# Kernel optimization log

Hardware: AMD Instinct MI355X
Metric: run time of the kernel (lower is better)

The kernel has to match this reference:

```python
import jax, jax.numpy as jnp
import numpy as np

B, G, F = 256, 2048, 128   # batch, graph_size, feat_size (== gcn_dim == k)
RNN_DIM = 512
K = F  # self.k = args.gcn_dim


def setup_inputs() -> dict:
    key = jax.random.key(0)
    k1, k2, k3 = jax.random.split(key, 3)
    node_embs = jax.random.normal(k1, (B, G, F), dtype=jnp.float32)
    mask = jnp.zeros((B, G), dtype=jnp.float32)
    h_t = jax.random.normal(k2, (B, RNN_DIM), dtype=jnp.float32)
    W_map = jax.random.normal(k3, (RNN_DIM, F), dtype=jnp.float32) * (1.0 / np.sqrt(RNN_DIM))
    b_map = jnp.zeros((F,), dtype=jnp.float32)
    return {"node_embs": node_embs, "mask": mask, "h_t": h_t, "W_map": W_map, "b_map": b_map}


def reference(node_embs, mask, h_t, W_map, b_map):
    # mapper: Linear + Tanh -> scorer [B, F]
    scorer = jnp.tanh(h_t @ W_map + b_map)
    # scores = bmm(node_embs, scorer) / ||scorer||  -> [B, G]
    norm = jnp.linalg.norm(scorer, axis=1, keepdims=True)  # [B, 1]
    scores = jnp.einsum('bgf,bf->bg', node_embs, scorer) / norm
    scores = scores + mask
    # top-k over graph dim (mask is all-zero so no -inf filtering/padding needed)
    vals, topk_indices = jax.lax.top_k(scores, K)  # [B, K]
    # gather node embeddings at topk indices, scale by tanh of gathered scores
    gathered = jnp.take_along_axis(node_embs, topk_indices[:, :, None], axis=1)  # [B, K, F]
    out = gathered * jnp.tanh(vals)[:, :, None]  # tanh(scores.gather) == tanh(vals)
    # log-softmax over graph dim, gather at topk, mean -> policy score [B]
    log_probs = jax.nn.log_softmax(scores, axis=-1)
    score = jnp.take_along_axis(log_probs, topk_indices, axis=-1)  # [B, K]
    policy_score = score.mean(axis=1)
    return (jnp.transpose(out, (0, 2, 1)), policy_score)  # ([B, F, K], [B])
```

## Files before the change

kernel.cpp:

```cpp
#include <hip/hip_runtime.h>
#include <cmath>

#define B_ 256
#define G_ 2048
#define F_ 128
#define RNN_ 512
#define K_ 128

__global__ __launch_bounds__(128) void k_scorer(const float* __restrict__ h_t,
                                                const float* __restrict__ W,
                                                const float* __restrict__ b_map,
                                                float* __restrict__ scorer_norm) {
    __shared__ float h[RNN_];
    __shared__ float red[128];
    const int b = blockIdx.x;
    const int f = threadIdx.x;
    for (int i = f; i < RNN_; i += 128) h[i] = h_t[b * RNN_ + i];
    __syncthreads();
    float acc = 0.f;
#pragma unroll 8
    for (int r = 0; r < RNN_; ++r) acc += h[r] * W[r * F_ + f];
    const float t = tanhf(acc + b_map[f]);
    red[f] = t * t;
    __syncthreads();
    for (int s = 64; s > 0; s >>= 1) {
        if (f < s) red[f] += red[f + s];
        __syncthreads();
    }
    const float norm = sqrtf(red[0]);
    scorer_norm[b * F_ + f] = t / norm;
}

__global__ __launch_bounds__(256) void k_scores(const float* __restrict__ node,
                                                const float* __restrict__ mask,
                                                const float* __restrict__ scorer_norm,
                                                float* __restrict__ scores) {
    const int b = blockIdx.y;
    const int gbase = blockIdx.x * 64;
    const int tid = threadIdx.x;
    const int wave = tid >> 6;
    const int lane = tid & 63;
    const int half = lane >> 5;
    const int l32 = lane & 31;

    const float4 s4 = ((const float4*)(scorer_norm + b * F_))[l32];
    const float4* nb = (const float4*)(node + (size_t)b * G_ * F_);
    const int rowbase = gbase + wave * 16;
#pragma unroll
    for (int p = 0; p < 8; ++p) {
        const int g = rowbase + p * 2 + half;
        const float4 e = nb[(size_t)g * 32 + l32];
        float part = e.x * s4.x + e.y * s4.y + e.z * s4.z + e.w * s4.w;
        part += __shfl_xor(part, 16);
        part += __shfl_xor(part, 8);
        part += __shfl_xor(part, 4);
        part += __shfl_xor(part, 2);
        part += __shfl_xor(part, 1);
        if (l32 == 0) scores[b * G_ + g] = part + mask[b * G_ + g];
    }
}

__global__ __launch_bounds__(512) void k_topk(const float* __restrict__ node,
                                              const float* __restrict__ scores,
                                              float* __restrict__ out,
                                              float* __restrict__ policy) {
    __shared__ float sc[G_];
    __shared__ unsigned long long keys[G_];
    __shared__ float tile[K_][33];
    __shared__ float tanhv[K_];
    __shared__ int idxk[K_];
    __shared__ float valk[K_];
    __shared__ float red[512];

    const int b = blockIdx.x;
    const int tid = threadIdx.x;

    for (int i = tid; i < G_; i += 512) {
        const float v = scores[b * G_ + i];
        sc[i] = v;
        unsigned u = __float_as_uint(v);
        u = (u & 0x80000000u) ? ~u : (u | 0x80000000u);
        keys[i] = ((unsigned long long)u << 32) | (unsigned)(G_ - 1 - i);
    }
    __syncthreads();

    for (int k = 2; k <= G_; k <<= 1) {
        for (int j = k >> 1; j > 0; j >>= 1) {
            for (int i = tid; i < G_; i += 512) {
                const int ij = i ^ j;
                if (ij > i) {
                    const unsigned long long a = keys[i], c = keys[ij];
                    const bool up = ((i & k) == 0);
                    if (up ? (a > c) : (a < c)) {
                        keys[i] = c;
                        keys[ij] = a;
                    }
                }
            }
            __syncthreads();
        }
    }

    if (tid < K_) {
        const unsigned long long key = keys[G_ - 1 - tid];
        const int idx = G_ - 1 - (int)(unsigned)(key & 0xFFFFFFFFull);
        idxk[tid] = idx;
        const float v = sc[idx];
        valk[tid] = v;
        tanhv[tid] = tanhf(v);
    }
    __syncthreads();

    const float maxv = sc[G_ - 1 - (int)(unsigned)(keys[G_ - 1] & 0xFFFFFFFFull)];
    float s = 0.f;
    for (int i = tid; i < G_; i += 512) s += expf(sc[i] - maxv);
    red[tid] = s;
    __syncthreads();
    for (int o = 256; o > 0; o >>= 1) {
        if (tid < o) red[tid] += red[tid + o];
        __syncthreads();
    }
    const float lse = maxv + logf(red[0]);
    if (tid == 0) {
        float sum = 0.f;
        for (int k2 = 0; k2 < K_; ++k2) sum += valk[k2];
        policy[b] = sum * (1.0f / K_) - lse;
    }

    const float* nb = node + (size_t)b * G_ * F_;
    float* ob = out + (size_t)b * F_ * K_;
    for (int f0 = 0; f0 < F_; f0 += 32) {
        for (int e = tid; e < K_ * 32; e += 512) {
            const int k2 = e >> 5;
            const int f = e & 31;
            tile[k2][f] = nb[(size_t)idxk[k2] * F_ + f0 + f];
        }
        __syncthreads();
        for (int e = tid; e < 32 * K_; e += 512) {
            const int f = e >> 7;
            const int k2 = e & 127;
            ob[(size_t)(f0 + f) * K_ + k2] = tile[k2][f] * tanhv[k2];
        }
        __syncthreads();
    }
}

extern "C" void kernel_launch(void* const* d_in, const int* in_sizes, int n_in,
                              void* d_out, int out_size, void* d_ws, size_t ws_size,
                              hipStream_t stream) {
    const float* node = (const float*)d_in[0];
    const float* mask = (const float*)d_in[1];
    const float* h_t = (const float*)d_in[2];
    const float* W = (const float*)d_in[3];
    const float* bm = (const float*)d_in[4];

    float* out = (float*)d_out;
    float* policy = out + (size_t)B_ * F_ * K_;

    float* scorer_norm = (float*)d_ws;
    float* scores = scorer_norm + B_ * F_;

    k_scorer<<<B_, 128, 0, stream>>>(h_t, W, bm, scorer_norm);
    k_scores<<<dim3(G_ / 64, B_), 256, 0, stream>>>(node, mask, scorer_norm, scores);
    k_topk<<<B_, 512, 0, stream>>>(node, scores, out, policy);
}
```

Measured before the change: 454.5 us.

## Replace full bitonic sort with radix-select threshold plus small sort of top-k

The top-k kernel no longer bitonic-sorts all 2048 keys. It runs an 8-pass radix select with per-wave shared histograms to find the exact k-th key, compacts the 128 winners with an atomic counter, and bitonic-sorts only those. The scorer kernel splits the RNN reduction across 512 threads in four partial sums, and the gather loads node rows as float4. The aim is to cut the O(G log² G) sort work and barriers, at the cost of eight histogram passes that each need several syncs.

```diff
diff --git a/kernel.cpp b/kernel.cpp
--- a/kernel.cpp
+++ b/kernel.cpp
@@ -7,28 +7,37 @@
 #define RNN_ 512
 #define K_ 128
 
-__global__ __launch_bounds__(128) void k_scorer(const float* __restrict__ h_t,
+__global__ __launch_bounds__(512) void k_scorer(const float* __restrict__ h_t,
                                                 const float* __restrict__ W,
                                                 const float* __restrict__ b_map,
                                                 float* __restrict__ scorer_norm) {
     __shared__ float h[RNN_];
-    __shared__ float red[128];
+    __shared__ float part[4][F_];
+    __shared__ float red[F_];
     const int b = blockIdx.x;
-    const int f = threadIdx.x;
-    for (int i = f; i < RNN_; i += 128) h[i] = h_t[b * RNN_ + i];
-    __syncthreads();
+    const int tid = threadIdx.x;
+    h[tid] = h_t[b * RNN_ + tid];
+    __syncthreads();
+    const int f = tid & 127;
+    const int qu = tid >> 7;
     float acc = 0.f;
+    const int r0 = qu * (RNN_ / 4);
 #pragma unroll 8
-    for (int r = 0; r < RNN_; ++r) acc += h[r] * W[r * F_ + f];
-    const float t = tanhf(acc + b_map[f]);
-    red[f] = t * t;
+    for (int r = r0; r < r0 + RNN_ / 4; ++r) acc += h[r] * W[r * F_ + f];
+    part[qu][f] = acc;
+    __syncthreads();
+    if (tid < F_) {
+        const float s = part[0][tid] + part[1][tid] + part[2][tid] + part[3][tid] + b_map[tid];
+        const float t = tanhf(s);
+        part[0][tid] = t;
+        red[tid] = t * t;
+    }
     __syncthreads();
     for (int s = 64; s > 0; s >>= 1) {
-        if (f < s) red[f] += red[f + s];
-        __syncthreads();
-    }
-    const float norm = sqrtf(red[0]);
-    scorer_norm[b * F_ + f] = t / norm;
+        if (tid < s) red[tid] += red[tid + s];
+        __syncthreads();
+    }
+    if (tid < F_) scorer_norm[b * F_ + tid] = part[0][tid] / sqrtf(red[0]);
 }
 
 __global__ __launch_bounds__(256) void k_scores(const float* __restrict__ node,
@@ -66,14 +75,20 @@
                                               float* __restrict__ policy) {
     __shared__ float sc[G_];
     __shared__ unsigned long long keys[G_];
+    __shared__ unsigned hist[8][256];
+    __shared__ unsigned long long win[K_];
     __shared__ float tile[K_][33];
     __shared__ float tanhv[K_];
     __shared__ int idxk[K_];
     __shared__ float valk[K_];
     __shared__ float red[512];
+    __shared__ unsigned long long prefix_sh;
+    __shared__ int need_sh;
+    __shared__ int cnt;
 
     const int b = blockIdx.x;
     const int tid = threadIdx.x;
+    const int w = tid >> 6;
 
     for (int i = tid; i < G_; i += 512) {
         const float v = scores[b * G_ + i];
@@ -82,18 +97,83 @@
         u = (u & 0x80000000u) ? ~u : (u | 0x80000000u);
         keys[i] = ((unsigned long long)u << 32) | (unsigned)(G_ - 1 - i);
     }
-    __syncthreads();
-
-    for (int k = 2; k <= G_; k <<= 1) {
+    if (tid == 0) cnt = 0;
+    __syncthreads();
+
+    unsigned long long prefix = 0;
+    int need = K_;
+    for (int shift = 56; shift >= 0; shift -= 8) {
+        for (int i = tid; i < 8 * 256; i += 512) ((unsigned*)hist)[i] = 0u;
+        __syncthreads();
+        const unsigned long long hi_mask =
+            (shift == 56) ? 0ull : (~0ull << (shift + 8));
+        for (int i = tid; i < G_; i += 512) {
+            const unsigned long long key = keys[i];
+            if ((key & hi_mask) == prefix)
+                atomicAdd(&hist[w][(unsigned)(key >> shift) & 255u], 1u);
+        }
+        __syncthreads();
+        if (tid < 256) {
+            unsigned s = 0;
+#pragma unroll
+            for (int ww = 0; ww < 8; ++ww) s += hist[ww][tid];
+            hist[0][tid] = s;
+        }
+        __syncthreads();
+        if (tid < 64) {
+            const int L = tid;
+            const unsigned h0 = hist[0][4 * L + 0];
+            const unsigned h1 = hist[0][4 * L + 1];
+            const unsigned h2 = hist[0][4 * L + 2];
+            const unsigned h3 = hist[0][4 * L + 3];
+            const unsigned s3 = h3, s2 = h2 + s3, s1 = h1 + s2, s0 = h0 + s1;
+            unsigned S = s0;
+            for (int off = 1; off < 64; off <<= 1) {
+                const unsigned t = __shfl_down(S, off);
+                if (L + off < 64) S += t;
+            }
+            unsigned Snext = __shfl_down(S, 1);
+            if (L == 63) Snext = 0;
+            const unsigned un = (unsigned)need;
+            const unsigned suf0 = Snext + s0, suf1 = Snext + s1;
+            const unsigned suf2 = Snext + s2, suf3 = Snext + s3, suf4 = Snext;
+            int d = -1;
+            unsigned sufd1 = 0;
+            if (suf0 >= un && suf1 < un) { d = 4 * L + 0; sufd1 = suf1; }
+            else if (suf1 >= un && suf2 < un) { d = 4 * L + 1; sufd1 = suf2; }
+            else if (suf2 >= un && suf3 < un) { d = 4 * L + 2; sufd1 = suf3; }
+            else if (suf3 >= un && suf4 < un) { d = 4 * L + 3; sufd1 = suf4; }
+            if (d >= 0) {
+                prefix_sh = prefix | ((unsigned long long)(unsigned)d << shift);
+                need_sh = need - (int)sufd1;
+            }
+        }
+        __syncthreads();
+        prefix = prefix_sh;
+        need = need_sh;
+    }
+    const unsigned long long T = prefix;
+
+    for (int i = tid; i < G_; i += 512) {
+        const unsigned long long key = keys[i];
+        if (key >= T) {
+            const int p = atomicAdd(&cnt, 1);
+            win[p] = key;
+        }
+    }
+    __syncthreads();
+
+    for (int k = 2; k <= K_; k <<= 1) {
         for (int j = k >> 1; j > 0; j >>= 1) {
-            for (int i = tid; i < G_; i += 512) {
+            if (tid < K_) {
+                const int i = tid;
                 const int ij = i ^ j;
                 if (ij > i) {
-                    const unsigned long long a = keys[i], c = keys[ij];
+                    const unsigned long long a = win[i], c = win[ij];
                     const bool up = ((i & k) == 0);
                     if (up ? (a > c) : (a < c)) {
-                        keys[i] = c;
-                        keys[ij] = a;
+                        win[i] = c;
+                        win[ij] = a;
                     }
                 }
             }
@@ -102,7 +182,7 @@
     }
 
     if (tid < K_) {
-        const unsigned long long key = keys[G_ - 1 - tid];
+        const unsigned long long key = win[K_ - 1 - tid];
         const int idx = G_ - 1 - (int)(unsigned)(key & 0xFFFFFFFFull);
         idxk[tid] = idx;
         const float v = sc[idx];
@@ -111,7 +191,7 @@
     }
     __syncthreads();
 
-    const float maxv = sc[G_ - 1 - (int)(unsigned)(keys[G_ - 1] & 0xFFFFFFFFull)];
+    const float maxv = valk[0];
     float s = 0.f;
     for (int i = tid; i < G_; i += 512) s += expf(sc[i] - maxv);
     red[tid] = s;
@@ -130,10 +210,14 @@
     const float* nb = node + (size_t)b * G_ * F_;
     float* ob = out + (size_t)b * F_ * K_;
     for (int f0 = 0; f0 < F_; f0 += 32) {
-        for (int e = tid; e < K_ * 32; e += 512) {
-            const int k2 = e >> 5;
-            const int f = e & 31;
-            tile[k2][f] = nb[(size_t)idxk[k2] * F_ + f0 + f];
+        for (int e = tid; e < K_ * 8; e += 512) {
+            const int k2 = e >> 3;
+            const int q = e & 7;
+            const float4 v = *(const float4*)(nb + (size_t)idxk[k2] * F_ + f0 + 4 * q);
+            tile[k2][4 * q + 0] = v.x;
+            tile[k2][4 * q + 1] = v.y;
+            tile[k2][4 * q + 2] = v.z;
+            tile[k2][4 * q + 3] = v.w;
         }
         __syncthreads();
         for (int e = tid; e < 32 * K_; e += 512) {
@@ -160,7 +244,7 @@
     float* scorer_norm = (float*)d_ws;
     float* scores = scorer_norm + B_ * F_;
 
-    k_scorer<<<B_, 128, 0, stream>>>(h_t, W, bm, scorer_norm);
+    k_scorer<<<B_, 512, 0, stream>>>(h_t, W, bm, scorer_norm);
     k_scores<<<dim3(G_ / 64, B_), 256, 0, stream>>>(node, mask, scorer_norm, scores);
     k_topk<<<B_, 512, 0, stream>>>(node, scores, out, policy);
 }
```

After: 398.6 us. 12.3% less time.

## Fuse scorer, scores and top-k into one kernel with radix select

Applied to the files above, without the earlier changes.

Merges the three kernels into one per-batch block. The scorer is computed in shared memory and the scores are kept in LDS instead of global memory. The full bitonic sort of 2048 keys is replaced by an 8-bit radix select over 64-bit keys, followed by a rank sort of the 128 winners. Gather loads are vectorised as float4. This removes launch overhead, the global scores round trip and many sort barriers, but it leaves only 256 blocks to stream the 256 MB of node embeddings, which may reduce the bandwidth the scores pass can reach.

```diff
diff --git a/kernel.cpp b/kernel.cpp
--- a/kernel.cpp
+++ b/kernel.cpp
@@ -7,133 +7,204 @@
 #define RNN_ 512
 #define K_ 128
 
-__global__ __launch_bounds__(128) void k_scorer(const float* __restrict__ h_t,
-                                                const float* __restrict__ W,
-                                                const float* __restrict__ b_map,
-                                                float* __restrict__ scorer_norm) {
+__global__ __launch_bounds__(512) void k_fused(const float* __restrict__ node,
+                                               const float* __restrict__ mask,
+                                               const float* __restrict__ h_t,
+                                               const float* __restrict__ W,
+                                               const float* __restrict__ b_map,
+                                               float* __restrict__ out,
+                                               float* __restrict__ policy) {
+    __shared__ float sc[G_];
+    __shared__ unsigned hist[2][8][256];
+    __shared__ unsigned long long win[K_];
+    __shared__ float tile[K_][33];
     __shared__ float h[RNN_];
-    __shared__ float red[128];
-    const int b = blockIdx.x;
-    const int f = threadIdx.x;
-    for (int i = f; i < RNN_; i += 128) h[i] = h_t[b * RNN_ + i];
-    __syncthreads();
-    float acc = 0.f;
-#pragma unroll 8
-    for (int r = 0; r < RNN_; ++r) acc += h[r] * W[r * F_ + f];
-    const float t = tanhf(acc + b_map[f]);
-    red[f] = t * t;
-    __syncthreads();
-    for (int s = 64; s > 0; s >>= 1) {
-        if (f < s) red[f] += red[f + s];
-        __syncthreads();
-    }
-    const float norm = sqrtf(red[0]);
-    scorer_norm[b * F_ + f] = t / norm;
-}
-
-__global__ __launch_bounds__(256) void k_scores(const float* __restrict__ node,
-                                                const float* __restrict__ mask,
-                                                const float* __restrict__ scorer_norm,
-                                                float* __restrict__ scores) {
-    const int b = blockIdx.y;
-    const int gbase = blockIdx.x * 64;
-    const int tid = threadIdx.x;
-    const int wave = tid >> 6;
-    const int lane = tid & 63;
-    const int half = lane >> 5;
-    const int l32 = lane & 31;
-
-    const float4 s4 = ((const float4*)(scorer_norm + b * F_))[l32];
-    const float4* nb = (const float4*)(node + (size_t)b * G_ * F_);
-    const int rowbase = gbase + wave * 16;
-#pragma unroll
-    for (int p = 0; p < 8; ++p) {
-        const int g = rowbase + p * 2 + half;
-        const float4 e = nb[(size_t)g * 32 + l32];
-        float part = e.x * s4.x + e.y * s4.y + e.z * s4.z + e.w * s4.w;
-        part += __shfl_xor(part, 16);
-        part += __shfl_xor(part, 8);
-        part += __shfl_xor(part, 4);
-        part += __shfl_xor(part, 2);
-        part += __shfl_xor(part, 1);
-        if (l32 == 0) scores[b * G_ + g] = part + mask[b * G_ + g];
-    }
-}
-
-__global__ __launch_bounds__(512) void k_topk(const float* __restrict__ node,
-                                              const float* __restrict__ scores,
-                                              float* __restrict__ out,
-                                              float* __restrict__ policy) {
-    __shared__ float sc[G_];
-    __shared__ unsigned long long keys[G_];
-    __shared__ float tile[K_][33];
+    __shared__ float part[4][F_];
+    __shared__ alignas(16) float snorm[F_];
     __shared__ float tanhv[K_];
     __shared__ int idxk[K_];
     __shared__ float valk[K_];
-    __shared__ float red[512];
+    __shared__ float red8[8];
+    __shared__ unsigned long long prefix_sh;
+    __shared__ int need_sh;
+    __shared__ int done_sh;
+    __shared__ int cnt;
 
     const int b = blockIdx.x;
     const int tid = threadIdx.x;
-
-    for (int i = tid; i < G_; i += 512) {
-        const float v = scores[b * G_ + i];
-        sc[i] = v;
-        unsigned u = __float_as_uint(v);
+    const int wv = tid >> 6;
+    const int lane = tid & 63;
+
+    for (int i = tid; i < 8 * 256; i += 512) ((unsigned*)hist[0])[i] = 0u;
+    if (tid == 0) { cnt = 0; done_sh = 0; }
+
+    h[tid] = h_t[b * RNN_ + tid];
+    __syncthreads();
+    {
+        const int f = tid & 127;
+        const int qu = tid >> 7;
+        float acc = 0.f;
+        const int r0 = qu * (RNN_ / 4);
+#pragma unroll 8
+        for (int r = r0; r < r0 + RNN_ / 4; ++r) acc += h[r] * W[r * F_ + f];
+        part[qu][f] = acc;
+    }
+    __syncthreads();
+    float tval = 0.f;
+    if (tid < F_)
+        tval = tanhf(part[0][tid] + part[1][tid] + part[2][tid] + part[3][tid] + b_map[tid]);
+    {
+        float v = tval * tval;
+#pragma unroll
+        for (int off = 32; off; off >>= 1) v += __shfl_xor(v, off);
+        if (lane == 0) red8[wv] = v;
+    }
+    __syncthreads();
+    if (tid == 0) {
+        float s = 0.f;
+#pragma unroll
+        for (int i = 0; i < 8; ++i) s += red8[i];
+        red8[0] = sqrtf(s);
+    }
+    __syncthreads();
+    if (tid < F_) snorm[tid] = tval / red8[0];
+    __syncthreads();
+
+    const int half = lane >> 5;
+    const int l32 = lane & 31;
+    const float4 s4 = *(const float4*)&snorm[l32 * 4];
+    const float4* nb = (const float4*)(node + (size_t)b * G_ * F_);
+    const int gstart = wv * 256 + half;
+#pragma unroll 4
+    for (int p = 0; p < 128; ++p) {
+        const int g = gstart + p * 2;
+        const float4 e = nb[(size_t)g * 32 + l32];
+        float d = e.x * s4.x + e.y * s4.y + e.z * s4.z + e.w * s4.w;
+        d += __shfl_xor(d, 16);
+        d += __shfl_xor(d, 8);
+        d += __shfl_xor(d, 4);
+        d += __shfl_xor(d, 2);
+        d += __shfl_xor(d, 1);
+        if (l32 == 0) sc[g] = d + mask[b * G_ + g];
+    }
+    __syncthreads();
+
+    unsigned long long kreg[4];
+#pragma unroll
+    for (int p = 0; p < 4; ++p) {
+        const int i = tid + p * 512;
+        unsigned u = __float_as_uint(sc[i]);
         u = (u & 0x80000000u) ? ~u : (u | 0x80000000u);
-        keys[i] = ((unsigned long long)u << 32) | (unsigned)(G_ - 1 - i);
-    }
-    __syncthreads();
-
-    for (int k = 2; k <= G_; k <<= 1) {
-        for (int j = k >> 1; j > 0; j >>= 1) {
-            for (int i = tid; i < G_; i += 512) {
-                const int ij = i ^ j;
-                if (ij > i) {
-                    const unsigned long long a = keys[i], c = keys[ij];
-                    const bool up = ((i & k) == 0);
-                    if (up ? (a > c) : (a < c)) {
-                        keys[i] = c;
-                        keys[ij] = a;
-                    }
-                }
+        kreg[p] = ((unsigned long long)u << 32) | (unsigned)(G_ - 1 - i);
+    }
+
+    unsigned long long prefix = 0ull;
+    int need = K_;
+    int round = 0;
+    for (int shift = 56; shift >= 0; shift -= 8, ++round) {
+        unsigned(*H)[256] = hist[round & 1];
+        const unsigned long long hi_mask = (shift == 56) ? 0ull : (~0ull << (shift + 8));
+#pragma unroll
+        for (int p = 0; p < 4; ++p) {
+            const unsigned long long key = kreg[p];
+            if ((key & hi_mask) == prefix)
+                atomicAdd(&H[wv][(unsigned)(key >> shift) & 255u], 1u);
+        }
+        __syncthreads();
+        if (wv == 0) {
+            const int L = lane;
+            unsigned h0 = 0, h1 = 0, h2 = 0, h3 = 0;
+#pragma unroll
+            for (int ww = 0; ww < 8; ++ww) {
+                h0 += H[ww][4 * L + 0];
+                h1 += H[ww][4 * L + 1];
+                h2 += H[ww][4 * L + 2];
+                h3 += H[ww][4 * L + 3];
             }
-            __syncthreads();
-        }
-    }
+            const unsigned s3 = h3, s2 = h2 + s3, s1 = h1 + s2, s0 = h0 + s1;
+            unsigned S = s0;
+            for (int off = 1; off < 64; off <<= 1) {
+                const unsigned tt = __shfl_down(S, off);
+                if (L + off < 64) S += tt;
+            }
+            unsigned Snext = __shfl_down(S, 1);
+            if (L == 63) Snext = 0;
+            const unsigned un = (unsigned)need;
+            const unsigned suf0 = Snext + s0, suf1 = Snext + s1;
+            const unsigned suf2 = Snext + s2, suf3 = Snext + s3, suf4 = Snext;
+            int d = -1;
+            unsigned sd = 0, sd1 = 0;
+            if (suf0 >= un && suf1 < un) { d = 4 * L + 0; sd = suf0; sd1 = suf1; }
+            else if (suf1 >= un && suf2 < un) { d = 4 * L + 1; sd = suf1; sd1 = suf2; }
+            else if (suf2 >= un && suf3 < un) { d = 4 * L + 2; sd = suf2; sd1 = suf3; }
+            else if (suf3 >= un && suf4 < un) { d = 4 * L + 3; sd = suf3; sd1 = suf4; }
+            if (d >= 0) {
+                prefix_sh = prefix | ((unsigned long long)(unsigned)d << shift);
+                need_sh = need - (int)sd1;
+                done_sh = (sd == un);
+            }
+        } else {
+            unsigned* Z = (unsigned*)hist[(round + 1) & 1];
+            for (int i = tid - 64; i < 8 * 256; i += 448) Z[i] = 0u;
+        }
+        __syncthreads();
+        prefix = prefix_sh;
+        need = need_sh;
+        if (done_sh) break;
+    }
+    const unsigned long long T = prefix;
+
+#pragma unroll
+    for (int p = 0; p < 4; ++p) {
+        if (kreg[p] >= T) {
+            const int q = atomicAdd(&cnt, 1);
+            if (q < K_) win[q] = kreg[p];
+        }
+    }
+    __syncthreads();
 
     if (tid < K_) {
-        const unsigned long long key = keys[G_ - 1 - tid];
-        const int idx = G_ - 1 - (int)(unsigned)(key & 0xFFFFFFFFull);
-        idxk[tid] = idx;
-        const float v = sc[idx];
-        valk[tid] = v;
-        tanhv[tid] = tanhf(v);
-    }
-    __syncthreads();
-
-    const float maxv = sc[G_ - 1 - (int)(unsigned)(keys[G_ - 1] & 0xFFFFFFFFull)];
+        const unsigned long long mykey = win[tid];
+        int rank = 0;
+#pragma unroll 8
+        for (int j = 0; j < K_; ++j) rank += (win[j] > mykey) ? 1 : 0;
+        const int idx = G_ - 1 - (int)(unsigned)(mykey & 0xFFFFFFFFull);
+        idxk[rank] = idx;
+        const float val = sc[idx];
+        valk[rank] = val;
+        tanhv[rank] = tanhf(val);
+    }
+    __syncthreads();
+
+    const float maxv = valk[0];
     float s = 0.f;
-    for (int i = tid; i < G_; i += 512) s += expf(sc[i] - maxv);
-    red[tid] = s;
-    __syncthreads();
-    for (int o = 256; o > 0; o >>= 1) {
-        if (tid < o) red[tid] += red[tid + o];
-        __syncthreads();
-    }
-    const float lse = maxv + logf(red[0]);
+#pragma unroll
+    for (int p = 0; p < 4; ++p) s += expf(sc[tid + p * 512] - maxv);
+#pragma unroll
+    for (int off = 32; off; off >>= 1) s += __shfl_xor(s, off);
+    if (lane == 0) red8[wv] = s;
+    __syncthreads();
     if (tid == 0) {
+        float tot = 0.f;
+#pragma unroll
+        for (int i = 0; i < 8; ++i) tot += red8[i];
+        const float lse = maxv + logf(tot);
         float sum = 0.f;
-        for (int k2 = 0; k2 < K_; ++k2) sum += valk[k2];
+        for (int k = 0; k < K_; ++k) sum += valk[k];
         policy[b] = sum * (1.0f / K_) - lse;
     }
 
-    const float* nb = node + (size_t)b * G_ * F_;
+    const float* nbase = node + (size_t)b * G_ * F_;
     float* ob = out + (size_t)b * F_ * K_;
     for (int f0 = 0; f0 < F_; f0 += 32) {
-        for (int e = tid; e < K_ * 32; e += 512) {
-            const int k2 = e >> 5;
-            const int f = e & 31;
-            tile[k2][f] = nb[(size_t)idxk[k2] * F_ + f0 + f];
+        for (int e = tid; e < K_ * 8; e += 512) {
+            const int k2 = e >> 3;
+            const int q = e & 7;
+            const float4 vv = *(const float4*)(nbase + (size_t)idxk[k2] * F_ + f0 + 4 * q);
+            tile[k2][4 * q + 0] = vv.x;
+            tile[k2][4 * q + 1] = vv.y;
+            tile[k2][4 * q + 2] = vv.z;
+            tile[k2][4 * q + 3] = vv.w;
         }
         __syncthreads();
         for (int e = tid; e < 32 * K_; e += 512) {
@@ -157,10 +228,5 @@
     float* out = (float*)d_out;
     float* policy = out + (size_t)B_ * F_ * K_;
 
-    float* scorer_norm = (float*)d_ws;
-    float* scores = scorer_norm + B_ * F_;
-
-    k_scorer<<<B_, 128, 0, stream>>>(h_t, W, bm, scorer_norm);
-    k_scores<<<dim3(G_ / 64, B_), 256, 0, stream>>>(node, mask, scorer_norm, scores);
-    k_topk<<<B_, 512, 0, stream>>>(node, scores, out, policy);
+    k_fused<<<B_, 512, 0, stream>>>(node, mask, h_t, W, bm, out, policy);
 }
```

Measured after the change: 473.8 us. 1.04x slower.
